# Performance work log

Hardware: AMD Instinct MI355X
Metric: run time of the kernel (lower is better)

The kernel has to match this reference:

```python
import jax, jax.numpy as jnp
import numpy as np

HEADS = 16
DIM_HEAD = 64
SCALE = DIM_HEAD ** -0.5
MASK_NEG = 1000000.0


def setup_inputs() -> dict:
    key = jax.random.key(0)
    ks = jax.random.split(key, 6)
    B, N, M, D = 2, 2048, 2048, 1024
    inner = HEADS * DIM_HEAD  # 1024
    x = jax.random.normal(ks[0], (B, N, D), dtype=jnp.float32)
    context = jax.random.normal(ks[1], (B, M, D), dtype=jnp.float32)
    mask = jax.random.randint(ks[2], (B, N), 0, 2, dtype=jnp.int32)
    Wq = jax.random.normal(ks[3], (D, inner), dtype=jnp.float32) * (D ** -0.5)
    Wkv = jax.random.normal(ks[4], (D, 2 * inner), dtype=jnp.float32) * (D ** -0.5)
    Wout = jax.random.normal(ks[5], (inner, D), dtype=jnp.float32) * (inner ** -0.5)
    bout = jnp.zeros((D,), dtype=jnp.float32)
    return {"x": x, "context": context, "mask": mask,
            "Wq": Wq, "Wkv": Wkv, "Wout": Wout, "bout": bout}


def _split_heads(t):
    # [b, n, (h d)] -> [b, h, n, d]
    b, n, _ = t.shape
    return t.reshape(b, n, HEADS, DIM_HEAD).transpose(0, 2, 1, 3)


def reference(x, context, mask, Wq, Wkv, Wout, bout):
    kv = context @ Wkv                      # [b, m, 2*inner]
    k, v = jnp.split(kv, 2, axis=-1)
    q = x @ Wq                              # [b, n, inner]
    q, k, v = _split_heads(q), _split_heads(k), _split_heads(v)
    dots = jnp.einsum('bhnd,bhmd->bhnm', q, k) * SCALE
    # mask is [b, n]: additive penalty per query row (faithful to source)
    dots = dots - (1.0 - mask.astype(jnp.float32))[:, None, :, None] * MASK_NEG
    attn = jax.nn.softmax(dots, axis=-1)
    out = jnp.einsum('bhnm,bhmd->bhnd', attn, v)  # [b, h, n, d]
    b, h, n, d = out.shape
    out = out.transpose(0, 2, 1, 3).reshape(b, n, h * d)
    return out @ Wout + bout
```

## Files before the change

kernel.cpp:

```cpp
#include <hip/hip_runtime.h>
#include <hip/hip_bf16.h>
#include <math.h>

#define BATCH   2
#define NQ      2048
#define NKV     2048
#define DMODEL  1024
#define HEADS   16
#define INNER   1024
#define KVCOLS  2048

typedef short bf16x8 __attribute__((ext_vector_type(8)));
typedef float f32x4  __attribute__((ext_vector_type(4)));

__device__ __forceinline__ short f2bf(float x) {
    __hip_bfloat16 h = __float2bfloat16(x);
    return *reinterpret_cast<short*>(&h);
}
__device__ __forceinline__ float bf2f(short h) {
    unsigned int u = ((unsigned int)(unsigned short)h) << 16;
    float f;
    __builtin_memcpy(&f, &u, 4);
    return f;
}
__device__ __forceinline__ void gl_lds16(const void* g, void* l) {
    __builtin_amdgcn_global_load_lds(
        (const __attribute__((address_space(1))) unsigned int*)g,
        (__attribute__((address_space(3))) unsigned int*)l, 16, 0, 0);
}
__device__ __forceinline__ int sw(int row, int chunk) {
    return row * 64 + ((chunk ^ (row & 7)) << 3);
}

__device__ __forceinline__ void split_chunk(const float* __restrict__ in,
                                            short* __restrict__ hi,
                                            short* __restrict__ lo, int id)
{
    const int i = (id * 256 + (int)threadIdx.x) * 4;
    float4 v = *(const float4*)(in + i);
    short4 h, l;
    h.x = f2bf(v.x); l.x = f2bf(v.x - bf2f(h.x));
    h.y = f2bf(v.y); l.y = f2bf(v.y - bf2f(h.y));
    h.z = f2bf(v.z); l.z = f2bf(v.z - bf2f(h.z));
    h.w = f2bf(v.w); l.w = f2bf(v.w - bf2f(h.w));
    *(short4*)(hi + i) = h;
    *(short4*)(lo + i) = l;
}

__device__ __forceinline__ void tile_transpose_split(
    const float* __restrict__ W, short* __restrict__ Wth, short* __restrict__ Wtl,
    int Kd, int Nd, int bx, int by, int split)
{
    __shared__ float t[32][33];
    const int lx = threadIdx.x & 31, ly = threadIdx.x >> 5;
    #pragma unroll
    for (int j = 0; j < 4; ++j)
        t[ly + j * 8][lx] = W[(size_t)(by * 32 + ly + j * 8) * Nd + bx * 32 + lx];
    __syncthreads();
    #pragma unroll
    for (int j = 0; j < 4; ++j) {
        const float v = t[lx][ly + j * 8];
        const short h = f2bf(v);
        const size_t idx = (size_t)(bx * 32 + ly + j * 8) * Kd + by * 32 + lx;
        Wth[idx] = h;
        if (split) Wtl[idx] = f2bf(v - bf2f(h));
    }
}

__global__ __launch_bounds__(256)
void prep_all(const float* __restrict__ x, const float* __restrict__ ctx,
              const float* __restrict__ Wq, const float* __restrict__ Wkv,
              const float* __restrict__ Wout,
              short* __restrict__ xh, short* __restrict__ xl,
              short* __restrict__ ch, short* __restrict__ cl,
              short* __restrict__ WqTh, short* __restrict__ WqTl,
              short* __restrict__ WkvTh, short* __restrict__ WkvTl,
              short* __restrict__ WoutT)
{
    const int id = blockIdx.x;
    if (id < 4096) {
        split_chunk(x, xh, xl, id);
    } else if (id < 8192) {
        split_chunk(ctx, ch, cl, id - 4096);
    } else {
        const int r = id - 8192;
        if (r < 1024)
            tile_transpose_split(Wq, WqTh, WqTl, 1024, 1024, r & 31, r >> 5, 1);
        else if (r < 3072)
            tile_transpose_split(Wkv, WkvTh, WkvTl, 1024, 2048, (r - 1024) & 63, (r - 1024) >> 6, 1);
        else
            tile_transpose_split(Wout, WoutT, nullptr, 1024, 1024, (r - 3072) & 31, (r - 3072) >> 5, 0);
    }
}

__global__ __launch_bounds__(256)
void qkv_gemm(const short* __restrict__ xh, const short* __restrict__ xl,
              const short* __restrict__ ch, const short* __restrict__ cl,
              const short* __restrict__ WqTh, const short* __restrict__ WqTl,
              const short* __restrict__ WkvTh, const short* __restrict__ WkvTl,
              short* __restrict__ qhp, short* __restrict__ qlp,
              short* __restrict__ khp, short* __restrict__ klp,
              short* __restrict__ vp)
{
    __shared__ short Ash[128 * 32];
    __shared__ short Asl[128 * 32];
    __shared__ short Bsh[128 * 32];
    __shared__ short Bsl[128 * 32];

    const int tid = threadIdx.x;
    const int z = blockIdx.z;
    const int m0 = blockIdx.y * 128, n0 = blockIdx.x * 128;
    const int w = tid >> 6, ln = tid & 63;
    const int wm = (w & 1) * 64, wn = (w >> 1) * 64;
    const int lr = ln & 15, lq = ln >> 4;
    const int terms = (z == 2) ? 1 : 3;

    const short* Ah  = (z == 0) ? xh : ch;
    const short* Al  = (z == 0) ? xl : cl;
    const short* Bth = (z == 0) ? WqTh : (z == 1 ? WkvTh : WkvTh + (size_t)1024 * 1024);
    const short* Btl = (z == 0) ? WqTl : WkvTl;

    f32x4 acc[4][4];
    #pragma unroll
    for (int mt = 0; mt < 4; ++mt)
        #pragma unroll
        for (int nt = 0; nt < 4; ++nt)
            #pragma unroll
            for (int r = 0; r < 4; ++r) acc[mt][nt][r] = 0.0f;

    for (int k0 = 0; k0 < 1024; k0 += 32) {
        __syncthreads();
        #pragma unroll
        for (int it = 0; it < 2; ++it) {
            const int f = it * 256 + tid;
            const int row = f >> 2, c = f & 3;
            const int cg = c ^ ((row >> 1) & 3);
            const size_t ao = (size_t)(m0 + row) * 1024 + k0 + cg * 8;
            const size_t bo = (size_t)(n0 + row) * 1024 + k0 + cg * 8;
            gl_lds16(Ah  + ao, Ash + f * 8);
            gl_lds16(Bth + bo, Bsh + f * 8);
            if (terms == 3) {
                gl_lds16(Al  + ao, Asl + f * 8);
                gl_lds16(Btl + bo, Bsl + f * 8);
            }
        }
        __syncthreads();

        bf16x8 ah[4], bh[4];
        #pragma unroll
        for (int t = 0; t < 4; ++t) {
            const int ar = wm + t * 16 + lr;
            const int br = wn + t * 16 + lr;
            ah[t] = *(const bf16x8*)(Ash + ar * 32 + ((lq ^ ((ar >> 1) & 3)) << 3));
            bh[t] = *(const bf16x8*)(Bsh + br * 32 + ((lq ^ ((br >> 1) & 3)) << 3));
        }
        #pragma unroll
        for (int mt = 0; mt < 4; ++mt)
            #pragma unroll
            for (int nt = 0; nt < 4; ++nt)
                acc[mt][nt] = __builtin_amdgcn_mfma_f32_16x16x32_bf16(
                    ah[mt], bh[nt], acc[mt][nt], 0, 0, 0);

        if (terms == 3) {
            bf16x8 al[4], bl[4];
            #pragma unroll
            for (int t = 0; t < 4; ++t) {
                const int ar = wm + t * 16 + lr;
                const int br = wn + t * 16 + lr;
                al[t] = *(const bf16x8*)(Asl + ar * 32 + ((lq ^ ((ar >> 1) & 3)) << 3));
                bl[t] = *(const bf16x8*)(Bsl + br * 32 + ((lq ^ ((br >> 1) & 3)) << 3));
            }
            #pragma unroll
            for (int mt = 0; mt < 4; ++mt)
                #pragma unroll
                for (int nt = 0; nt < 4; ++nt) {
                    acc[mt][nt] = __builtin_amdgcn_mfma_f32_16x16x32_bf16(
                        ah[mt], bl[nt], acc[mt][nt], 0, 0, 0);
                    acc[mt][nt] = __builtin_amdgcn_mfma_f32_16x16x32_bf16(
                        al[mt], bh[nt], acc[mt][nt], 0, 0, 0);
                }
        }
    }

    const float scale = (z == 0) ? 2.0f : 1.0f;
    short* Chi = (z == 0) ? qhp : (z == 1 ? khp : vp);
    short* Clo = (z == 0) ? qlp : klp;
    #pragma unroll
    for (int mt = 0; mt < 4; ++mt)
        #pragma unroll
        for (int nt = 0; nt < 4; ++nt)
            #pragma unroll
            for (int r = 0; r < 4; ++r) {
                const int row = m0 + wm + mt * 16 + lq * 4 + r;
                const int col = n0 + wn + nt * 16 + lr;
                const float v = acc[mt][nt][r] * scale;
                const short hh = f2bf(v);
                Chi[(size_t)row * 1024 + col] = hh;
                if (z != 2)
                    Clo[(size_t)row * 1024 + col] = f2bf(v - bf2f(hh));
            }
}

__global__ __launch_bounds__(256)
void gemm_out(const short* __restrict__ A, const short* __restrict__ Bt,
              float* __restrict__ C, const float* __restrict__ bias)
{
    __shared__ short As[128 * 64];
    __shared__ short Bs[64 * 64];
    const int tid = threadIdx.x;
    const int m0 = blockIdx.y * 128, n0 = blockIdx.x * 64;
    const int w = tid >> 6, ln = tid & 63;
    const int wm = (w & 1) * 64, wn = (w >> 1) * 32;
    const int lr = ln & 15, lq = ln >> 4;

    f32x4 acc[4][2];
    #pragma unroll
    for (int mt = 0; mt < 4; ++mt)
        #pragma unroll
        for (int nt = 0; nt < 2; ++nt)
            #pragma unroll
            for (int r = 0; r < 4; ++r) acc[mt][nt][r] = 0.0f;

    for (int k0 = 0; k0 < 1024; k0 += 64) {
        __syncthreads();
        #pragma unroll
        for (int it = 0; it < 4; ++it) {
            const int f = it * 256 + tid;
            const int row = f >> 3, c8 = f & 7;
            const int cg = c8 ^ (row & 7);
            gl_lds16(A + (size_t)(m0 + row) * 1024 + k0 + cg * 8, As + f * 8);
        }
        #pragma unroll
        for (int it = 0; it < 2; ++it) {
            const int f = it * 256 + tid;
            const int row = f >> 3, c8 = f & 7;
            const int cg = c8 ^ (row & 7);
            gl_lds16(Bt + (size_t)(n0 + row) * 1024 + k0 + cg * 8, Bs + f * 8);
        }
        __syncthreads();
        #pragma unroll
        for (int ks = 0; ks < 2; ++ks) {
            bf16x8 af[4], bfr[2];
            #pragma unroll
            for (int t = 0; t < 4; ++t) {
                const int ar = wm + t * 16 + lr;
                af[t] = *(const bf16x8*)(As + ar * 64 + (((ks * 4 + lq) ^ (ar & 7)) << 3));
            }
            #pragma unroll
            for (int t = 0; t < 2; ++t) {
                const int br = wn + t * 16 + lr;
                bfr[t] = *(const bf16x8*)(Bs + br * 64 + (((ks * 4 + lq) ^ (br & 7)) << 3));
            }
            #pragma unroll
            for (int mt = 0; mt < 4; ++mt)
                #pragma unroll
                for (int nt = 0; nt < 2; ++nt)
                    acc[mt][nt] = __builtin_amdgcn_mfma_f32_16x16x32_bf16(
                        af[mt], bfr[nt], acc[mt][nt], 0, 0, 0);
        }
    }
    #pragma unroll
    for (int mt = 0; mt < 4; ++mt)
        #pragma unroll
        for (int nt = 0; nt < 2; ++nt)
            #pragma unroll
            for (int r = 0; r < 4; ++r) {
                const int row = m0 + wm + mt * 16 + lq * 4 + r;
                const int col = n0 + wn + nt * 16 + lr;
                C[(size_t)row * 1024 + col] = acc[mt][nt][r] + bias[col];
            }
}

__device__ __forceinline__ void vwrite(int* __restrict__ vt32, int dg4, int kp32,
                                       int2 a, int2 b)
{
    const short* as = (const short*)&a;
    const short* bs = (const short*)&b;
    #pragma unroll
    for (int j = 0; j < 4; ++j)
        vt32[(dg4 + j) * 32 + (((kp32 >> 2) ^ ((dg4 + j) & 7)) << 2) + (kp32 & 3)] =
            (int)((unsigned short)as[j] | ((unsigned int)(unsigned short)bs[j] << 16));
}

__global__ __launch_bounds__(256, 2)
void flash_v8(const short* __restrict__ qh, const short* __restrict__ ql,
              const short* __restrict__ kh, const short* __restrict__ kl,
              const short* __restrict__ vp, const int* __restrict__ mask,
              short* __restrict__ aob)
{
    const int qt = blockIdx.x, h = blockIdx.y, b = blockIdx.z;
    const int tid = threadIdx.x;
    const int w = tid >> 6, ln = tid & 63;
    const int lr = ln & 15, lq = ln >> 4;

    __shared__ short Kh[2 * 4096];
    __shared__ short Kl[2 * 4096];
    __shared__ short Vt[2 * 4096];
    __shared__ short Ps[128 * 64];

    const size_t qrow0 = (size_t)(b * NQ + qt * 128);

    bf16x8 aqh[2][2], aql[2][2];
    #pragma unroll
    for (int m = 0; m < 2; ++m)
        #pragma unroll
        for (int ks = 0; ks < 2; ++ks) {
            const size_t qoff = (qrow0 + w * 32 + m * 16 + lr) * INNER + h * 64 + ks * 32 + lq * 8;
            aqh[m][ks] = *(const bf16x8*)(qh + qoff);
            aql[m][ks] = *(const bf16x8*)(ql + qoff);
        }
    float bmag[2][4];
    #pragma unroll
    for (int m = 0; m < 2; ++m)
        #pragma unroll
        for (int r = 0; r < 4; ++r)
            bmag[m][r] = mask[b * NQ + qt * 128 + w * 32 + m * 16 + lq * 4 + r]
                         ? 0.0f : 12582912.0f;

    bf16x8 vone;
    #pragma unroll
    for (int j = 0; j < 8; ++j) vone[j] = (short)0x3F80;

    size_t koff[2];
    #pragma unroll
    for (int it = 0; it < 2; ++it) {
        const int f = it * 256 + tid;
        const int krow = f >> 3, kc = f & 7;
        const int kcg = kc ^ (krow & 7);
        koff[it] = ((size_t)(b * NKV + krow)) * INNER + h * 64 + kcg * 8;
    }

    const int idx = tid & 31;
    const int vj  = (idx & 15) + ((idx >> 4) << 5);
    const int kp32 = (idx & 15) * 2 + (idx >> 4);
    const int dgA = (tid >> 5) * 4;
    const int dgB = dgA + 32;
    int2 rva, rvb, rvc, rvd;

    {
        const short* v0 = vp + (size_t)(b * NKV + vj) * INNER + h * 64;
        rva = *(const int2*)(v0 + dgA);
        rvb = *(const int2*)(v0 + dgA + 16 * INNER);
        rvc = *(const int2*)(v0 + dgB);
        rvd = *(const int2*)(v0 + dgB + 16 * INNER);
        gl_lds16(kh + koff[0], Kh + tid * 8);
        gl_lds16(kh + koff[1], Kh + 2048 + tid * 8);
        gl_lds16(kl + koff[0], Kl + tid * 8);
        gl_lds16(kl + koff[1], Kl + 2048 + tid * 8);
        int* vt32 = (int*)Vt;
        vwrite(vt32, dgA, kp32, rva, rvb);
        vwrite(vt32, dgB, kp32, rvc, rvd);
    }

    f32x4 oacc[2][4];
    #pragma unroll
    for (int m = 0; m < 2; ++m)
        #pragma unroll
        for (int dg = 0; dg < 4; ++dg)
            #pragma unroll
            for (int r = 0; r < 4; ++r) oacc[m][dg][r] = 0.0f;
    f32x4 pacc[2];
    #pragma unroll
    for (int m = 0; m < 2; ++m)
        #pragma unroll
        for (int r = 0; r < 4; ++r) pacc[m][r] = 0.0f;

    const float C16 = 1.44269504f * 0.0625f;

    for (int kt = 0; kt < NKV / 64; ++kt) {
        const int cur = kt & 1;
        __syncthreads();

        if (kt < NKV / 64 - 1) {
            const size_t kadd = (size_t)((kt + 1) * 64) * INNER;
            const short* v0 = vp + (size_t)(b * NKV + (kt + 1) * 64 + vj) * INNER + h * 64;
            rva = *(const int2*)(v0 + dgA);
            rvb = *(const int2*)(v0 + dgA + 16 * INNER);
            rvc = *(const int2*)(v0 + dgB);
            rvd = *(const int2*)(v0 + dgB + 16 * INNER);
            const int nb = (cur ^ 1) * 4096;
            gl_lds16(kh + koff[0] + kadd, Kh + nb + tid * 8);
            gl_lds16(kh + koff[1] + kadd, Kh + nb + 2048 + tid * 8);
            gl_lds16(kl + koff[0] + kadd, Kl + nb + tid * 8);
            gl_lds16(kl + koff[1] + kadd, Kl + nb + 2048 + tid * 8);
        }

        const short* KhC = Kh + cur * 4096;
        const short* KlC = Kl + cur * 4096;
        const short* VtC = Vt + cur * 4096;

        f32x4 sacc[2][4];
        #pragma unroll
        for (int m = 0; m < 2; ++m)
            #pragma unroll
            for (int g = 0; g < 4; ++g)
                #pragma unroll
                for (int r = 0; r < 4; ++r) sacc[m][g][r] = 0.0f;
        #pragma unroll
        for (int ks = 0; ks < 2; ++ks) {
            #pragma unroll
            for (int g = 0; g < 4; ++g) {
                const bf16x8 bkh = *(const bf16x8*)(KhC + sw(g * 16 + lr, ks * 4 + lq));
                const bf16x8 bkl = *(const bf16x8*)(KlC + sw(g * 16 + lr, ks * 4 + lq));
                #pragma unroll
                for (int m = 0; m < 2; ++m) {
                    sacc[m][g] = __builtin_amdgcn_mfma_f32_16x16x32_bf16(aqh[m][ks], bkh, sacc[m][g], 0, 0, 0);
                    sacc[m][g] = __builtin_amdgcn_mfma_f32_16x16x32_bf16(aqh[m][ks], bkl, sacc[m][g], 0, 0, 0);
                    sacc[m][g] = __builtin_amdgcn_mfma_f32_16x16x32_bf16(aql[m][ks], bkh, sacc[m][g], 0, 0, 0);
                }
            }
        }

        #pragma unroll
        for (int m = 0; m < 2; ++m)
            #pragma unroll
            for (int r = 0; r < 4; ++r) {
                const int prow = w * 32 + m * 16 + lq * 4 + r;
                short4 pw;
                #pragma unroll
                for (int g = 0; g < 4; ++g) {
                    const float sq = (sacc[m][g][r] + bmag[m][r]) - bmag[m][r];
                    const float xx = sq * C16;
                    float pv;
                    asm("v_exp_f32 %0, %1" : "=v"(pv) : "v"(xx));
                    ((short*)&pw)[g] = f2bf(pv);
                }
                *(short4*)(Ps + sw(prow, lr >> 1) + (lr & 1) * 4) = pw;
            }

        #pragma unroll
        for (int ks = 0; ks < 2; ++ks) {
            bf16x8 ap[2];
            #pragma unroll
            for (int m = 0; m < 2; ++m) {
                ap[m] = *(const bf16x8*)(Ps + sw(w * 32 + m * 16 + lr, ks * 4 + lq));
                pacc[m] = __builtin_amdgcn_mfma_f32_16x16x32_bf16(ap[m], vone, pacc[m], 0, 0, 0);
            }
            #pragma unroll
            for (int dg = 0; dg < 4; ++dg) {
                const bf16x8 bv = *(const bf16x8*)(VtC + sw(dg * 16 + lr, ks * 4 + lq));
                oacc[0][dg] = __builtin_amdgcn_mfma_f32_16x16x32_bf16(ap[0], bv, oacc[0][dg], 0, 0, 0);
                oacc[1][dg] = __builtin_amdgcn_mfma_f32_16x16x32_bf16(ap[1], bv, oacc[1][dg], 0, 0, 0);
            }
        }

        if (kt < NKV / 64 - 1) {
            int* vt32 = (int*)(Vt + (cur ^ 1) * 4096);
            vwrite(vt32, dgA, kp32, rva, rvb);
            vwrite(vt32, dgB, kp32, rvc, rvd);
        }
    }

    #pragma unroll
    for (int m = 0; m < 2; ++m) {
        float pinv[4];
        #pragma unroll
        for (int r = 0; r < 4; ++r) pinv[r] = 1.0f / pacc[m][r];
        #pragma unroll
        for (int dg = 0; dg < 4; ++dg)
            #pragma unroll
            for (int r = 0; r < 4; ++r) {
                const int row = w * 32 + m * 16 + lq * 4 + r;
                aob[(qrow0 + row) * INNER + h * 64 + dg * 16 + lr] =
                    f2bf(oacc[m][dg][r] * pinv[r]);
            }
    }
}

extern "C" void kernel_launch(void* const* d_in, const int* in_sizes, int n_in,
                              void* d_out, int out_size, void* d_ws, size_t ws_size,
                              hipStream_t stream)
{
    const float* x    = (const float*)d_in[0];
    const float* ctx  = (const float*)d_in[1];
    const int*   mask = (const int*)d_in[2];
    const float* Wq   = (const float*)d_in[3];
    const float* Wkv  = (const float*)d_in[4];
    const float* Wout = (const float*)d_in[5];
    const float* bout = (const float*)d_in[6];
    float* out = (float*)d_out;

    short* base  = (short*)d_ws;
    short* xh    = base;
    short* xl    = base + (size_t)4 * 1024 * 1024;
    short* aob   = xh;
    short* WqTh  = base + (size_t) 8 * 1024 * 1024;
    short* WqTl  = base + (size_t) 9 * 1024 * 1024;
    short* qhp   = base + (size_t)10 * 1024 * 1024;
    short* qlp   = base + (size_t)14 * 1024 * 1024;
    short* WkvTh = base + (size_t)18 * 1024 * 1024;
    short* WkvTl = base + (size_t)20 * 1024 * 1024;
    short* khp   = base + (size_t)22 * 1024 * 1024;
    short* klp   = base + (size_t)26 * 1024 * 1024;
    short* WoutT = base + (size_t)30 * 1024 * 1024;
    short* ch    = base + (size_t)31 * 1024 * 1024;
    short* cl    = base + (size_t)35 * 1024 * 1024;
    short* vp    = base + (size_t)39 * 1024 * 1024;

    const dim3 blk(256);
    prep_all<<<12288, blk, 0, stream>>>(x, ctx, Wq, Wkv, Wout,
                                        xh, xl, ch, cl,
                                        WqTh, WqTl, WkvTh, WkvTl, WoutT);
    qkv_gemm<<<dim3(8, 32, 3), blk, 0, stream>>>(
        xh, xl, ch, cl, WqTh, WqTl, WkvTh, WkvTl,
        qhp, qlp, khp, klp, vp);
    flash_v8<<<dim3(NQ / 128, HEADS, BATCH), dim3(256), 0, stream>>>(
        qhp, qlp, khp, klp, vp, mask, aob);
    gemm_out<<<dim3(1024 / 64, 4096 / 128), blk, 0, stream>>>(
        aob, WoutT, out, bout);
}
```

Before: 270.0 us.

## Split each KV tile across two waves per query group in flash kernel

The flash attention kernel goes from 256 to 512 threads per block. Each pair of waves shares a 32-row query slice and splits the 64 keys of every KV tile, so each wave does half the QK and PV MFMAs. The partial output and row-sum accumulators are combined through LDS at the end. This aims to raise occupancy and latency hiding and to spread the tile loads over more threads. In exchange, each wave reloads Q fragments, the kernel needs a final cross-wave reduction with extra barriers, and the 512-thread blocks put more pressure on registers.

After: 275.3 us. Within noise of the previous version (+2.0%).

```diff
diff --git a/kernel.cpp b/kernel.cpp
--- a/kernel.cpp
+++ b/kernel.cpp
@@ -271,19 +271,19 @@
             }
 }
 
-__device__ __forceinline__ void vwrite(int* __restrict__ vt32, int dg4, int kp32,
+__device__ __forceinline__ void vwrite(int* __restrict__ vt32, int dg4, int slot,
                                        int2 a, int2 b)
 {
     const short* as = (const short*)&a;
     const short* bs = (const short*)&b;
     #pragma unroll
     for (int j = 0; j < 4; ++j)
-        vt32[(dg4 + j) * 32 + (((kp32 >> 2) ^ ((dg4 + j) & 7)) << 2) + (kp32 & 3)] =
+        vt32[(dg4 + j) * 32 + (((slot >> 2) ^ ((dg4 + j) & 7)) << 2) + (slot & 3)] =
             (int)((unsigned short)as[j] | ((unsigned int)(unsigned short)bs[j] << 16));
 }
 
-__global__ __launch_bounds__(256, 2)
-void flash_v8(const short* __restrict__ qh, const short* __restrict__ ql,
+__global__ __launch_bounds__(512, 4)
+void flash_v9(const short* __restrict__ qh, const short* __restrict__ ql,
               const short* __restrict__ kh, const short* __restrict__ kl,
               const short* __restrict__ vp, const int* __restrict__ mask,
               short* __restrict__ aob)
@@ -292,11 +292,13 @@
     const int tid = threadIdx.x;
     const int w = tid >> 6, ln = tid & 63;
     const int lr = ln & 15, lq = ln >> 4;
-
-    __shared__ short Kh[2 * 4096];
-    __shared__ short Kl[2 * 4096];
-    __shared__ short Vt[2 * 4096];
-    __shared__ short Ps[128 * 64];
+    const int kw = w & 1, wq = w >> 1;
+
+    __shared__ short lds[32768];
+    short* Kh = lds;
+    short* Kl = lds + 8192;
+    short* Vt = lds + 16384;
+    short* Ps = lds + 24576;
 
     const size_t qrow0 = (size_t)(b * NQ + qt * 128);
 
@@ -305,7 +307,7 @@
     for (int m = 0; m < 2; ++m)
         #pragma unroll
         for (int ks = 0; ks < 2; ++ks) {
-            const size_t qoff = (qrow0 + w * 32 + m * 16 + lr) * INNER + h * 64 + ks * 32 + lq * 8;
+            const size_t qoff = (qrow0 + wq * 32 + m * 16 + lr) * INNER + h * 64 + ks * 32 + lq * 8;
             aqh[m][ks] = *(const bf16x8*)(qh + qoff);
             aql[m][ks] = *(const bf16x8*)(ql + qoff);
         }
@@ -314,42 +316,28 @@
     for (int m = 0; m < 2; ++m)
         #pragma unroll
         for (int r = 0; r < 4; ++r)
-            bmag[m][r] = mask[b * NQ + qt * 128 + w * 32 + m * 16 + lq * 4 + r]
+            bmag[m][r] = mask[b * NQ + qt * 128 + wq * 32 + m * 16 + lq * 4 + r]
                          ? 0.0f : 12582912.0f;
 
     bf16x8 vone;
     #pragma unroll
     for (int j = 0; j < 8; ++j) vone[j] = (short)0x3F80;
 
-    size_t koff[2];
-    #pragma unroll
-    for (int it = 0; it < 2; ++it) {
-        const int f = it * 256 + tid;
-        const int krow = f >> 3, kc = f & 7;
-        const int kcg = kc ^ (krow & 7);
-        koff[it] = ((size_t)(b * NKV + krow)) * INNER + h * 64 + kcg * 8;
-    }
-
-    const int idx = tid & 31;
+    const int krow = tid >> 3, kc = tid & 7;
+    const int kcg = kc ^ (krow & 7);
+    const size_t koff0 = ((size_t)(b * NKV + krow)) * INNER + h * 64 + kcg * 8;
+
+    const int idx = tid & 31, dg4 = (tid >> 5) * 4;
     const int vj  = (idx & 15) + ((idx >> 4) << 5);
-    const int kp32 = (idx & 15) * 2 + (idx >> 4);
-    const int dgA = (tid >> 5) * 4;
-    const int dgB = dgA + 32;
-    int2 rva, rvb, rvc, rvd;
+    int2 rva, rvb;
 
     {
-        const short* v0 = vp + (size_t)(b * NKV + vj) * INNER + h * 64;
-        rva = *(const int2*)(v0 + dgA);
-        rvb = *(const int2*)(v0 + dgA + 16 * INNER);
-        rvc = *(const int2*)(v0 + dgB);
-        rvd = *(const int2*)(v0 + dgB + 16 * INNER);
-        gl_lds16(kh + koff[0], Kh + tid * 8);
-        gl_lds16(kh + koff[1], Kh + 2048 + tid * 8);
-        gl_lds16(kl + koff[0], Kl + tid * 8);
-        gl_lds16(kl + koff[1], Kl + 2048 + tid * 8);
-        int* vt32 = (int*)Vt;
-        vwrite(vt32, dgA, kp32, rva, rvb);
-        vwrite(vt32, dgB, kp32, rvc, rvd);
+        const short* v0 = vp + (size_t)(b * NKV + vj) * INNER + h * 64 + dg4;
+        rva = *(const int2*)(v0);
+        rvb = *(const int2*)(v0 + 16 * INNER);
+        gl_lds16(kh + koff0, Kh + tid * 8);
+        gl_lds16(kl + koff0, Kl + tid * 8);
+        vwrite((int*)Vt, dg4, idx, rva, rvb);
     }
 
     f32x4 oacc[2][4];
@@ -366,6 +354,7 @@
         for (int r = 0; r < 4; ++r) pacc[m][r] = 0.0f;
 
     const float C16 = 1.44269504f * 0.0625f;
+    const int wbase = w * 1024;
 
     for (int kt = 0; kt < NKV / 64; ++kt) {
         const int cur = kt & 1;
@@ -373,35 +362,32 @@
 
         if (kt < NKV / 64 - 1) {
             const size_t kadd = (size_t)((kt + 1) * 64) * INNER;
-            const short* v0 = vp + (size_t)(b * NKV + (kt + 1) * 64 + vj) * INNER + h * 64;
-            rva = *(const int2*)(v0 + dgA);
-            rvb = *(const int2*)(v0 + dgA + 16 * INNER);
-            rvc = *(const int2*)(v0 + dgB);
-            rvd = *(const int2*)(v0 + dgB + 16 * INNER);
+            const short* v0 = vp + (size_t)(b * NKV + (kt + 1) * 64 + vj) * INNER + h * 64 + dg4;
+            rva = *(const int2*)(v0);
+            rvb = *(const int2*)(v0 + 16 * INNER);
             const int nb = (cur ^ 1) * 4096;
-            gl_lds16(kh + koff[0] + kadd, Kh + nb + tid * 8);
-            gl_lds16(kh + koff[1] + kadd, Kh + nb + 2048 + tid * 8);
-            gl_lds16(kl + koff[0] + kadd, Kl + nb + tid * 8);
-            gl_lds16(kl + koff[1] + kadd, Kl + nb + 2048 + tid * 8);
+            gl_lds16(kh + koff0 + kadd, Kh + nb + tid * 8);
+            gl_lds16(kl + koff0 + kadd, Kl + nb + tid * 8);
         }
 
         const short* KhC = Kh + cur * 4096;
         const short* KlC = Kl + cur * 4096;
         const short* VtC = Vt + cur * 4096;
 
-        f32x4 sacc[2][4];
+        f32x4 sacc[2][2];
         #pragma unroll
         for (int m = 0; m < 2; ++m)
             #pragma unroll
-            for (int g = 0; g < 4; ++g)
+            for (int g = 0; g < 2; ++g)
                 #pragma unroll
                 for (int r = 0; r < 4; ++r) sacc[m][g][r] = 0.0f;
         #pragma unroll
         for (int ks = 0; ks < 2; ++ks) {
             #pragma unroll
-            for (int g = 0; g < 4; ++g) {
-                const bf16x8 bkh = *(const bf16x8*)(KhC + sw(g * 16 + lr, ks * 4 + lq));
-                const bf16x8 bkl = *(const bf16x8*)(KlC + sw(g * 16 + lr, ks * 4 + lq));
+            for (int g = 0; g < 2; ++g) {
+                const int gg = kw * 2 + g;
+                const bf16x8 bkh = *(const bf16x8*)(KhC + sw(gg * 16 + lr, ks * 4 + lq));
+                const bf16x8 bkl = *(const bf16x8*)(KlC + sw(gg * 16 + lr, ks * 4 + lq));
                 #pragma unroll
                 for (int m = 0; m < 2; ++m) {
                     sacc[m][g] = __builtin_amdgcn_mfma_f32_16x16x32_bf16(aqh[m][ks], bkh, sacc[m][g], 0, 0, 0);
@@ -415,55 +401,78 @@
         for (int m = 0; m < 2; ++m)
             #pragma unroll
             for (int r = 0; r < 4; ++r) {
-                const int prow = w * 32 + m * 16 + lq * 4 + r;
-                short4 pw;
-                #pragma unroll
-                for (int g = 0; g < 4; ++g) {
+                const int row32 = m * 16 + lq * 4 + r;
+                unsigned int pw = 0;
+                #pragma unroll
+                for (int g = 0; g < 2; ++g) {
                     const float sq = (sacc[m][g][r] + bmag[m][r]) - bmag[m][r];
                     const float xx = sq * C16;
                     float pv;
                     asm("v_exp_f32 %0, %1" : "=v"(pv) : "v"(xx));
-                    ((short*)&pw)[g] = f2bf(pv);
+                    pw |= ((unsigned int)(unsigned short)f2bf(pv)) << (g * 16);
                 }
-                *(short4*)(Ps + sw(prow, lr >> 1) + (lr & 1) * 4) = pw;
-            }
-
-        #pragma unroll
-        for (int ks = 0; ks < 2; ++ks) {
-            bf16x8 ap[2];
+                const int addr = wbase + row32 * 32 +
+                                 (((lr >> 2) ^ ((row32 >> 1) & 3)) << 3) + (lr & 3) * 2;
+                *(int*)(Ps + addr) = (int)pw;
+            }
+
+        bf16x8 ap[2];
+        #pragma unroll
+        for (int m = 0; m < 2; ++m) {
+            const int row = m * 16 + lr;
+            ap[m] = *(const bf16x8*)(Ps + wbase + row * 32 +
+                                     ((lq ^ ((row >> 1) & 3)) << 3));
+            pacc[m] = __builtin_amdgcn_mfma_f32_16x16x32_bf16(ap[m], vone, pacc[m], 0, 0, 0);
+        }
+        #pragma unroll
+        for (int dg = 0; dg < 4; ++dg) {
+            const bf16x8 bv = *(const bf16x8*)(VtC + sw(dg * 16 + lr, kw * 4 + lq));
+            oacc[0][dg] = __builtin_amdgcn_mfma_f32_16x16x32_bf16(ap[0], bv, oacc[0][dg], 0, 0, 0);
+            oacc[1][dg] = __builtin_amdgcn_mfma_f32_16x16x32_bf16(ap[1], bv, oacc[1][dg], 0, 0, 0);
+        }
+
+        if (kt < NKV / 64 - 1) {
+            vwrite((int*)(Vt + (cur ^ 1) * 4096), dg4, idx, rva, rvb);
+        }
+    }
+
+    __syncthreads();
+    {
+        float* scr = (float*)lds;
+        float* slot = scr + ((size_t)(wq * 64 + ln)) * 40;
+        if (kw) {
             #pragma unroll
             for (int m = 0; m < 2; ++m) {
-                ap[m] = *(const bf16x8*)(Ps + sw(w * 32 + m * 16 + lr, ks * 4 + lq));
-                pacc[m] = __builtin_amdgcn_mfma_f32_16x16x32_bf16(ap[m], vone, pacc[m], 0, 0, 0);
-            }
-            #pragma unroll
-            for (int dg = 0; dg < 4; ++dg) {
-                const bf16x8 bv = *(const bf16x8*)(VtC + sw(dg * 16 + lr, ks * 4 + lq));
-                oacc[0][dg] = __builtin_amdgcn_mfma_f32_16x16x32_bf16(ap[0], bv, oacc[0][dg], 0, 0, 0);
-                oacc[1][dg] = __builtin_amdgcn_mfma_f32_16x16x32_bf16(ap[1], bv, oacc[1][dg], 0, 0, 0);
-            }
-        }
-
-        if (kt < NKV / 64 - 1) {
-            int* vt32 = (int*)(Vt + (cur ^ 1) * 4096);
-            vwrite(vt32, dgA, kp32, rva, rvb);
-            vwrite(vt32, dgB, kp32, rvc, rvd);
-        }
-    }
-
-    #pragma unroll
-    for (int m = 0; m < 2; ++m) {
-        float pinv[4];
-        #pragma unroll
-        for (int r = 0; r < 4; ++r) pinv[r] = 1.0f / pacc[m][r];
-        #pragma unroll
-        for (int dg = 0; dg < 4; ++dg)
-            #pragma unroll
-            for (int r = 0; r < 4; ++r) {
-                const int row = w * 32 + m * 16 + lq * 4 + r;
-                aob[(qrow0 + row) * INNER + h * 64 + dg * 16 + lr] =
-                    f2bf(oacc[m][dg][r] * pinv[r]);
-            }
+                #pragma unroll
+                for (int dg = 0; dg < 4; ++dg)
+                    *(f32x4*)(slot + m * 16 + dg * 4) = oacc[m][dg];
+                *(f32x4*)(slot + 32 + m * 4) = pacc[m];
+            }
+        }
+        __syncthreads();
+        if (!kw) {
+            #pragma unroll
+            for (int m = 0; m < 2; ++m) {
+                #pragma unroll
+                for (int dg = 0; dg < 4; ++dg)
+                    oacc[m][dg] += *(const f32x4*)(slot + m * 16 + dg * 4);
+                pacc[m] += *(const f32x4*)(slot + 32 + m * 4);
+            }
+            #pragma unroll
+            for (int m = 0; m < 2; ++m) {
+                float pinv[4];
+                #pragma unroll
+                for (int r = 0; r < 4; ++r) pinv[r] = 1.0f / pacc[m][r];
+                #pragma unroll
+                for (int dg = 0; dg < 4; ++dg)
+                    #pragma unroll
+                    for (int r = 0; r < 4; ++r) {
+                        const int row = wq * 32 + m * 16 + lq * 4 + r;
+                        aob[(qrow0 + row) * INNER + h * 64 + dg * 16 + lr] =
+                            f2bf(oacc[m][dg][r] * pinv[r]);
+                    }
+            }
+        }
     }
 }
 
@@ -504,7 +513,7 @@
     qkv_gemm<<<dim3(8, 32, 3), blk, 0, stream>>>(
         xh, xl, ch, cl, WqTh, WqTl, WkvTh, WkvTl,
         qhp, qlp, khp, klp, vp);
-    flash_v8<<<dim3(NQ / 128, HEADS, BATCH), dim3(256), 0, stream>>>(
+    flash_v9<<<dim3(NQ / 128, HEADS, BATCH), dim3(512), 0, stream>>>(
         qhp, qlp, khp, klp, vp, mask, aob);
     gemm_out<<<dim3(1024 / 64, 4096 / 128), blk, 0, stream>>>(
         aob, WoutT, out, bout);
```
